# Kernel optimization log

Measured on AMD Instinct MI355X. Metric: run time of the kernel, lower is better.

Reference implementation:

```python
import jax, jax.numpy as jnp
import numpy as np

BN_EPS = 1e-5
W_SCALE = 0.05  # keep pre-softmax logits in a sane range with random weights


def setup_inputs() -> dict:
    key = jax.random.key(0)
    ks = jax.random.split(key, 8)
    b, C, H, W = 2, 512, 80, 80
    Ck, Cv, Co = 256, 256, 512
    return {
        "x": jax.random.normal(ks[0], (b, C, H, W), dtype=jnp.float32),
        "wk": jax.random.normal(ks[1], (Ck, C), dtype=jnp.float32) * W_SCALE,
        "bk": jax.random.normal(ks[2], (Ck,), dtype=jnp.float32) * W_SCALE,
        "gamma": jnp.ones((Ck,), dtype=jnp.float32),
        "beta": jnp.zeros((Ck,), dtype=jnp.float32),
        "rmean": jnp.zeros((Ck,), dtype=jnp.float32),
        "rvar": jnp.ones((Ck,), dtype=jnp.float32),
        "wv": jax.random.normal(ks[3], (Cv, C), dtype=jnp.float32) * W_SCALE,
        "bv": jax.random.normal(ks[4], (Cv,), dtype=jnp.float32) * W_SCALE,
        "wW": jax.random.normal(ks[5], (Co, Cv), dtype=jnp.float32) * W_SCALE,
        "bW": jax.random.normal(ks[6], (Co,), dtype=jnp.float32) * W_SCALE,
    }


def reference(x, wk, bk, gamma, beta, rmean, rvar, wv, bv, wW, bW):
    b, C, H, Wd = x.shape
    N = H * Wd
    Ck = wk.shape[0]
    Cv = wv.shape[0]
    # f_key == f_query (shared module): 1x1 conv + BN(inference) + ReLU
    k = jnp.einsum('bchw,oc->bohw', x, wk) + bk[:, None, None]
    scale_bn = gamma / jnp.sqrt(rvar + BN_EPS)
    k = (k - rmean[:, None, None]) * scale_bn[:, None, None] + beta[:, None, None]
    k = jax.nn.relu(k).reshape(b, Ck, N)          # [b, Ck, N]
    q = jnp.transpose(k, (0, 2, 1))               # [b, N, Ck] (query shares weights with key)
    # f_value: plain 1x1 conv
    v = (jnp.einsum('bchw,oc->bohw', x, wv) + bv[:, None, None]).reshape(b, Cv, N)
    sim = jnp.einsum('bnc,bcm->bnm', q, k) * (Ck ** -0.5)  # [b, N, N]
    sim = jax.nn.softmax(sim, axis=-1)
    ctx = jnp.einsum('bnm,bvm->bvn', sim, v).reshape(b, Cv, H, Wd)
    out = jnp.einsum('bvhw,ov->bohw', ctx, wW) + bW[:, None, None]
    return out
```

## Files before the change

kernel.cpp:

```cpp
#include <hip/hip_runtime.h>
#include <stdint.h>

typedef __attribute__((ext_vector_type(8))) short bf16x8;
typedef __attribute__((ext_vector_type(4))) float f32x4;

__device__ __forceinline__ ushort f2bf(float f) {
    union { float f; uint32_t i; } v; v.f = f;
    uint32_t r = v.i + 0x7fff + ((v.i >> 16) & 1);
    return (ushort)(r >> 16);
}
__device__ __forceinline__ uint32_t cvtpk(float lo, float hi) {
    uint32_t r;
    asm("v_cvt_pk_bf16_f32 %0, %1, %2" : "=v"(r) : "v"(lo), "v"(hi));
    return r;
}

typedef unsigned int uint_as1 __attribute__((address_space(1)));
typedef unsigned int uint_as3 __attribute__((address_space(3)));
__device__ __forceinline__ void async16(const void* g, void* l) {
    __builtin_amdgcn_global_load_lds((const uint_as1*)g, (uint_as3*)l, 16, 0, 0);
}


__global__ void cvt_f32_bf16(const float* __restrict__ in, ushort* __restrict__ out, int n) {
    int i = blockIdx.x * blockDim.x + threadIdx.x;
    if (i < n) out[i] = f2bf(in[i]);
}

__global__ void prep_bn(const float* __restrict__ bk, const float* __restrict__ gamma,
                        const float* __restrict__ beta, const float* __restrict__ rmean,
                        const float* __restrict__ rvar,
                        float* __restrict__ scaleA, float* __restrict__ shiftA) {
    int i = threadIdx.x;
    float s = gamma[i] * rsqrtf(rvar[i] + 1e-5f);
    scaleA[i] = 0.25f * s;
    shiftA[i] = 0.25f * ((bk[i] - rmean[i]) * s + beta[i]);
}

__global__ void transpose_cvt(const float* __restrict__ x, ushort* __restrict__ xt) {
    __shared__ float t[32][33];
    int b = blockIdx.z;
    int n0 = blockIdx.x * 32, c0 = blockIdx.y * 32;
    const float* xb = x + (size_t)b * 512 * 6400;
    ushort* xtb = xt + (size_t)b * 6400 * 512;
    int tx = threadIdx.x, ty = threadIdx.y;
    t[ty][tx] = xb[(size_t)(c0 + ty) * 6400 + n0 + tx];
    __syncthreads();
    xtb[(size_t)(n0 + ty) * 512 + c0 + tx] = f2bf(t[tx][ty]);
}

template <int EPI>
__global__ __launch_bounds__(256) void gemm_nt(
    const ushort* __restrict__ A, const ushort* __restrict__ B, void* __restrict__ Cout,
    int K, int lda, int ldb, int ldc,
    size_t zsa, size_t zsb, size_t zsc,
    const float* __restrict__ vec0, const float* __restrict__ vec1) {
    __shared__ __align__(16) ushort smem[6 * 4096];

    A += (size_t)blockIdx.z * zsa;
    B += (size_t)blockIdx.z * zsb;

    const int tid = threadIdx.x;
    const int lane = tid & 63, wave = tid >> 6;
    const int wm = wave & 1, wn = wave >> 1;
    const int bM = blockIdx.y * 128, bN = blockIdx.x * 128;

    const int sr = lane >> 2;
    const int sc = (lane & 3) * 8;
    const ushort* gA0 = A + (size_t)(bM + wave * 32 + sr) * lda + sc;
    const ushort* gA1 = gA0 + (size_t)16 * lda;
    const ushort* gB0 = B + (size_t)(bN + wave * 32 + sr) * ldb + sc;
    const ushort* gB1 = gB0 + (size_t)16 * ldb;
    ushort* lAw = &smem[wave * 1024];
    ushort* lBw = &smem[3 * 4096 + wave * 1024];

    const int rowA = wm * 64;
    const int rowB = wn * 64;
    const int fr = lane & 15;
    const int fk = (lane >> 4) * 8;

    f32x4 acc[4][4] = {};
    const int nT = K >> 5;

    auto stage = [&](int t, int buf) {
        const int k0 = t * 32;
        const int ob = buf * 4096;
        async16(gA0 + k0, lAw + ob);
        async16(gA1 + k0, lAw + ob + 512);
        async16(gB0 + k0, lBw + ob);
        async16(gB1 + k0, lBw + ob + 512);
    };

    stage(0, 0);
    if (nT > 1) stage(1, 1);

    for (int t = 0; t < nT; ++t) {
        if (t + 1 < nT) { asm volatile("s_waitcnt vmcnt(4)" ::: "memory"); }
        else            { asm volatile("s_waitcnt vmcnt(0)" ::: "memory"); }
        __builtin_amdgcn_sched_barrier(0);
        __builtin_amdgcn_s_barrier();
        __builtin_amdgcn_sched_barrier(0);
        if (t + 2 < nT) stage(t + 2, (t + 2) % 3);
        const int cur = t % 3;
        const ushort* lA = &smem[cur * 4096];
        const ushort* lB = &smem[3 * 4096 + cur * 4096];
        bf16x8 af[4], bff[4];
#pragma unroll
        for (int mi = 0; mi < 4; mi++)
            af[mi] = *(const bf16x8*)&lA[(rowA + mi * 16 + fr) * 32 + fk];
#pragma unroll
        for (int ni = 0; ni < 4; ni++)
            bff[ni] = *(const bf16x8*)&lB[(rowB + ni * 16 + fr) * 32 + fk];
#pragma unroll
        for (int mi = 0; mi < 4; mi++)
#pragma unroll
            for (int ni = 0; ni < 4; ni++)
                acc[mi][ni] = __builtin_amdgcn_mfma_f32_16x16x32_bf16(af[mi], bff[ni], acc[mi][ni], 0, 0, 0);
        __builtin_amdgcn_sched_barrier(0);
    }
    __builtin_amdgcn_s_barrier();
    __builtin_amdgcn_sched_barrier(0);

    float* Cf = (float*)Cout + (size_t)blockIdx.z * zsc;
    ushort* Cu = (ushort*)Cout + (size_t)blockIdx.z * zsc;
    float* lt = (float*)smem;
    const int g4 = (lane >> 4) * 4;
    const int cl = lane & 15;
    const int lr = tid >> 3;
    const int ch = tid & 7;

#pragma unroll
    for (int mi = 0; mi < 4; ++mi) {
#pragma unroll
        for (int ni = 0; ni < 4; ++ni) {
            const int lcol = wn * 64 + ni * 16 + cl;
#pragma unroll
            for (int r = 0; r < 4; ++r)
                lt[(wm * 16 + g4 + r) * 132 + lcol] = acc[mi][ni][r];
        }
        __syncthreads();
        {
            const int brow = (lr < 16) ? (mi * 16 + lr) : (64 + mi * 16 + (lr - 16));
            const int grow = bM + brow;
            const int gcol = bN + ch * 16;
            float vv[16];
#pragma unroll
            for (int i = 0; i < 16; i += 4) {
                f32x4 q = *(const f32x4*)&lt[lr * 132 + ch * 16 + i];
                vv[i] = q[0]; vv[i + 1] = q[1]; vv[i + 2] = q[2]; vv[i + 3] = q[3];
            }
            if (EPI == 1) {
#pragma unroll
                for (int i = 0; i < 16; i++)
                    vv[i] = fmaxf(vv[i] * vec0[gcol + i] + vec1[gcol + i], 0.f);
            }
            if (EPI == 2 || EPI == 3) {
                const float rb = vec0[grow];
#pragma unroll
                for (int i = 0; i < 16; i++) vv[i] += rb;
            }
            if (EPI == 3) {
#pragma unroll
                for (int i = 0; i < 16; i += 4) {
                    f32x4 q = { vv[i], vv[i + 1], vv[i + 2], vv[i + 3] };
                    *(f32x4*)&Cf[(size_t)grow * ldc + gcol + i] = q;
                }
            } else {
                uint4 q0 = { cvtpk(vv[0], vv[1]), cvtpk(vv[2], vv[3]),
                             cvtpk(vv[4], vv[5]), cvtpk(vv[6], vv[7]) };
                uint4 q1 = { cvtpk(vv[8], vv[9]), cvtpk(vv[10], vv[11]),
                             cvtpk(vv[12], vv[13]), cvtpk(vv[14], vv[15]) };
                *(uint4*)&Cu[(size_t)grow * ldc + gcol] = q0;
                *(uint4*)&Cu[(size_t)grow * ldc + gcol + 8] = q1;
            }
        }
        __syncthreads();
    }
}

template <int EPI>
__global__ __launch_bounds__(256) void gemm_wide(
    const ushort* __restrict__ A, const ushort* __restrict__ B, void* __restrict__ Cout,
    int K, int lda, int ldb, int ldc,
    size_t zsa, size_t zsb, size_t zsc,
    float* __restrict__ rsum) {
    __shared__ __align__(16) ushort smem[3 * 4096 + 3 * 8192];

    A += (size_t)blockIdx.z * zsa;
    B += (size_t)blockIdx.z * zsb;

    const int tid = threadIdx.x;
    const int lane = tid & 63, wave = tid >> 6;
    const int wm = wave & 1, wn = wave >> 1;
    const int bM = blockIdx.y * 128, bN = blockIdx.x * 256;

    const int sr = lane >> 2;
    const int scs = ((lane & 3) ^ ((lane >> 3) & 3)) * 8;
    const ushort* gA0 = A + (size_t)(bM + wave * 32 + sr) * lda + scs;
    const ushort* gA1 = gA0 + (size_t)16 * lda;
    const ushort* gB0 = B + (size_t)(bN + wave * 64 + sr) * ldb + scs;
    const ushort* gB1 = gB0 + (size_t)16 * ldb;
    const ushort* gB2 = gB0 + (size_t)32 * ldb;
    const ushort* gB3 = gB0 + (size_t)48 * ldb;
    ushort* lAw = &smem[wave * 1024];
    ushort* lBw = &smem[3 * 4096 + wave * 2048];

    const int rowA = wm * 64;
    const int rowB = wn * 128;
    const int fr = lane & 15;
    const int fq = lane >> 4;
    const int fk = (fq ^ ((fr >> 1) & 3)) * 8;

    f32x4 acc[4][8] = {};
    const int nT = K >> 5;

    auto stage = [&](int t, int buf) {
        const int k0 = t * 32;
        ushort* la = lAw + buf * 4096;
        ushort* lb = lBw + buf * 8192;
        async16(gA0 + k0, la);
        async16(gA1 + k0, la + 512);
        async16(gB0 + k0, lb);
        async16(gB1 + k0, lb + 512);
        async16(gB2 + k0, lb + 1024);
        async16(gB3 + k0, lb + 1536);
    };

    stage(0, 0);
    if (nT > 1) stage(1, 1);

    for (int t = 0; t < nT; ++t) {
        if (t + 1 < nT) { asm volatile("s_waitcnt vmcnt(6)" ::: "memory"); }
        else            { asm volatile("s_waitcnt vmcnt(0)" ::: "memory"); }
        __builtin_amdgcn_sched_barrier(0);
        __builtin_amdgcn_s_barrier();
        __builtin_amdgcn_sched_barrier(0);
        if (t + 2 < nT) stage(t + 2, (t + 2) % 3);
        const int cur = t % 3;
        const ushort* lA = &smem[cur * 4096];
        const ushort* lB = &smem[3 * 4096 + cur * 8192];
        bf16x8 af[4], bff[8];
#pragma unroll
        for (int mi = 0; mi < 4; mi++)
            af[mi] = *(const bf16x8*)&lA[(rowA + mi * 16 + fr) * 32 + fk];
#pragma unroll
        for (int ni = 0; ni < 8; ni++)
            bff[ni] = *(const bf16x8*)&lB[(rowB + ni * 16 + fr) * 32 + fk];
#pragma unroll
        for (int mi = 0; mi < 4; mi++)
#pragma unroll
            for (int ni = 0; ni < 8; ni++)
                acc[mi][ni] = __builtin_amdgcn_mfma_f32_16x16x32_bf16(af[mi], bff[ni], acc[mi][ni], 0, 0, 0);
        __builtin_amdgcn_sched_barrier(0);
    }
    __builtin_amdgcn_s_barrier();
    __builtin_amdgcn_sched_barrier(0);

    float* Cf = (float*)Cout + (size_t)blockIdx.z * zsc;
    ushort* Cu = (ushort*)Cout + (size_t)blockIdx.z * zsc;
    float* lt = (float*)smem;
    const int g4 = fq * 4;
    const int cl = fr;
    const int lr = tid >> 3;
    const int ch = tid & 7;

#pragma unroll
    for (int mi = 0; mi < 4; ++mi) {
#pragma unroll
        for (int ni = 0; ni < 8; ++ni) {
            const int lcol = wn * 128 + ni * 16 + cl;
#pragma unroll
            for (int r = 0; r < 4; ++r)
                lt[(wm * 16 + g4 + r) * 260 + lcol] = acc[mi][ni][r];
        }
        __syncthreads();
        {
            const int brow = (lr < 16) ? (mi * 16 + lr) : (64 + mi * 16 + (lr - 16));
            const int grow = bM + brow;
            float vv[32];
#pragma unroll
            for (int h = 0; h < 2; ++h)
#pragma unroll
                for (int i = 0; i < 16; i += 4) {
                    f32x4 q = *(const f32x4*)&lt[lr * 260 + h * 128 + ch * 16 + i];
                    vv[h * 16 + i] = q[0]; vv[h * 16 + i + 1] = q[1];
                    vv[h * 16 + i + 2] = q[2]; vv[h * 16 + i + 3] = q[3];
                }
            if (EPI == 5) {
                float ssum = 0.f;
#pragma unroll
                for (int i = 0; i < 32; i++) { vv[i] = __expf(vv[i]); ssum += vv[i]; }
                ssum += __shfl_down(ssum, 4, 8);
                ssum += __shfl_down(ssum, 2, 8);
                ssum += __shfl_down(ssum, 1, 8);
                if (ch == 0) rsum[(size_t)blockIdx.x * 6400 + grow] = ssum;
#pragma unroll
                for (int h = 0; h < 2; ++h) {
                    const int gcol = bN + h * 128 + ch * 16;
                    const float* p = &vv[h * 16];
                    uint4 q0 = { cvtpk(p[0], p[1]), cvtpk(p[2], p[3]),
                                 cvtpk(p[4], p[5]), cvtpk(p[6], p[7]) };
                    uint4 q1 = { cvtpk(p[8], p[9]), cvtpk(p[10], p[11]),
                                 cvtpk(p[12], p[13]), cvtpk(p[14], p[15]) };
                    *(uint4*)&Cu[(size_t)grow * ldc + gcol] = q0;
                    *(uint4*)&Cu[(size_t)grow * ldc + gcol + 8] = q1;
                }
            } else {
#pragma unroll
                for (int h = 0; h < 2; ++h) {
                    const int gcol = bN + h * 128 + ch * 16;
#pragma unroll
                    for (int i = 0; i < 16; i += 4) {
                        f32x4 q = { vv[h * 16 + i], vv[h * 16 + i + 1],
                                    vv[h * 16 + i + 2], vv[h * 16 + i + 3] };
                        *(f32x4*)&Cf[(size_t)grow * ldc + gcol + i] = q;
                    }
                }
            }
        }
        __syncthreads();
    }
}

__global__ __launch_bounds__(256) void combine_inv(const float* __restrict__ rsum,
                                                   float* __restrict__ inv) {
    int r = blockIdx.x * 256 + threadIdx.x;
    float s = 0.f;
#pragma unroll
    for (int xb = 0; xb < 25; xb++) s += rsum[(size_t)xb * 6400 + r];
    inv[r] = 1.f / s;
}

__global__ __launch_bounds__(256) void reduce_ctx(const float* __restrict__ part, ushort* __restrict__ ctx,
                                                  const float* __restrict__ inv) {
    const size_t CH = 1638400;
    size_t i = ((size_t)blockIdx.x * 256 + threadIdx.x) * 4;
    float4 a = *(const float4*)&part[i];
#pragma unroll
    for (int c = 1; c < 10; c++) {
        float4 s = *(const float4*)&part[i + (size_t)c * CH];
        a.x += s.x; a.y += s.y; a.z += s.z; a.w += s.w;
    }
    const float w = inv[i >> 8];
    uint2 o = { cvtpk(a.x * w, a.y * w), cvtpk(a.z * w, a.w * w) };
    *(uint2*)&ctx[i] = o;
}

extern "C" void kernel_launch(void* const* d_in, const int* in_sizes, int n_in,
                              void* d_out, int out_size, void* d_ws, size_t ws_size,
                              hipStream_t stream) {
    (void)in_sizes; (void)n_in; (void)out_size; (void)ws_size;
    const float* x     = (const float*)d_in[0];
    const float* wk    = (const float*)d_in[1];
    const float* bk    = (const float*)d_in[2];
    const float* gamma = (const float*)d_in[3];
    const float* beta  = (const float*)d_in[4];
    const float* rmean = (const float*)d_in[5];
    const float* rvar  = (const float*)d_in[6];
    const float* wv    = (const float*)d_in[7];
    const float* bv    = (const float*)d_in[8];
    const float* wW    = (const float*)d_in[9];
    const float* bW    = (const float*)d_in[10];
    float* out = (float*)d_out;

    ushort* Xt   = (ushort*)d_ws;
    ushort* wkb  = Xt + 6553600;
    ushort* wvb  = wkb + 131072;
    ushort* wWb  = wvb + 131072;
    ushort* Kt   = wWb + 131072;
    ushort* V    = Kt + 3276800;
    ushort* ctxT = V + 3276800;
    ushort* S    = ctxT + 3276800;
    float* scaleA = (float*)(S + 40960000);
    float* shiftA = scaleA + 256;
    float* rowsum = shiftA + 256;
    float* inv    = rowsum + 160000;
    float* part   = inv + 6400;

    cvt_f32_bf16<<<512, 256, 0, stream>>>(wk, wkb, 131072);
    cvt_f32_bf16<<<512, 256, 0, stream>>>(wv, wvb, 131072);
    cvt_f32_bf16<<<512, 256, 0, stream>>>(wW, wWb, 131072);
    prep_bn<<<1, 256, 0, stream>>>(bk, gamma, beta, rmean, rvar, scaleA, shiftA);
    transpose_cvt<<<dim3(200, 16, 2), dim3(32, 32), 0, stream>>>(x, Xt);

    gemm_nt<1><<<dim3(2, 50, 2), 256, 0, stream>>>(Xt, wkb, Kt, 512, 512, 512, 256,
                                                   3276800, 0, 1638400, scaleA, shiftA);
    gemm_nt<2><<<dim3(50, 2, 2), 256, 0, stream>>>(wvb, Xt, V, 512, 512, 512, 6400,
                                                   0, 3276800, 1638400, bv, nullptr);

    for (int b = 0; b < 2; b++) {
        ushort* Ktb  = Kt + (size_t)b * 1638400;
        ushort* Vb   = V  + (size_t)b * 1638400;
        ushort* ctxb = ctxT + (size_t)b * 1638400;
        gemm_wide<5><<<dim3(25, 50), 256, 0, stream>>>(Ktb, Ktb, S, 256, 256, 256, 6400,
                                                       0, 0, 0, rowsum);
        combine_inv<<<25, 256, 0, stream>>>(rowsum, inv);
        gemm_wide<4><<<dim3(1, 50, 10), 256, 0, stream>>>(S, Vb, part, 640, 6400, 6400, 256,
                                                          640, 640, 1638400, nullptr);
        reduce_ctx<<<1600, 256, 0, stream>>>(part, ctxb, inv);
    }

    gemm_nt<3><<<dim3(50, 4, 2), 256, 0, stream>>>(wWb, ctxT, out, 256, 256, 256, 6400,
                                                   0, 1638400, 3276800, bW, nullptr);
}
```

Measured before the change: 338.1 us.

## Fuse QK^T, exp and PV into one flash-style kernel, drop S buffer

New measurement: 312.5 us. 7.6% less time.

```diff
diff --git a/kernel.cpp b/kernel.cpp
--- a/kernel.cpp
+++ b/kernel.cpp
@@ -66,10 +66,10 @@
     const int bM = blockIdx.y * 128, bN = blockIdx.x * 128;
 
     const int sr = lane >> 2;
-    const int sc = (lane & 3) * 8;
-    const ushort* gA0 = A + (size_t)(bM + wave * 32 + sr) * lda + sc;
+    const int scs = ((lane & 3) ^ ((lane >> 3) & 3)) * 8;
+    const ushort* gA0 = A + (size_t)(bM + wave * 32 + sr) * lda + scs;
     const ushort* gA1 = gA0 + (size_t)16 * lda;
-    const ushort* gB0 = B + (size_t)(bN + wave * 32 + sr) * ldb + sc;
+    const ushort* gB0 = B + (size_t)(bN + wave * 32 + sr) * ldb + scs;
     const ushort* gB1 = gB0 + (size_t)16 * ldb;
     ushort* lAw = &smem[wave * 1024];
     ushort* lBw = &smem[3 * 4096 + wave * 1024];
@@ -77,7 +77,7 @@
     const int rowA = wm * 64;
     const int rowB = wn * 64;
     const int fr = lane & 15;
-    const int fk = (lane >> 4) * 8;
+    const int fk = ((lane >> 4) ^ ((fr >> 1) & 3)) * 8;
 
     f32x4 acc[4][4] = {};
     const int nT = K >> 5;
@@ -178,147 +178,208 @@
     }
 }
 
-template <int EPI>
-__global__ __launch_bounds__(256) void gemm_wide(
-    const ushort* __restrict__ A, const ushort* __restrict__ B, void* __restrict__ Cout,
-    int K, int lda, int ldb, int ldc,
-    size_t zsa, size_t zsb, size_t zsc,
+__global__ __launch_bounds__(256, 2) void fused_spv(
+    const ushort* __restrict__ Kt,
+    const ushort* __restrict__ V,
+    float* __restrict__ part,
     float* __restrict__ rsum) {
-    __shared__ __align__(16) ushort smem[3 * 4096 + 3 * 8192];
-
-    A += (size_t)blockIdx.z * zsa;
-    B += (size_t)blockIdx.z * zsb;
+    __shared__ __align__(16) ushort smem[40960];
+
+    const ushort* Ktb = Kt + (size_t)blockIdx.z * 1638400;
+    const ushort* Vb  = V  + (size_t)blockIdx.z * 1638400;
+    float* partb = part + (size_t)blockIdx.z * 8192000;
+    float* rsumb = rsum + (size_t)blockIdx.z * 32000;
 
     const int tid = threadIdx.x;
     const int lane = tid & 63, wave = tid >> 6;
     const int wm = wave & 1, wn = wave >> 1;
-    const int bM = blockIdx.y * 128, bN = blockIdx.x * 256;
+    const int mc = blockIdx.x;
+    const int bM = blockIdx.y * 128;
 
     const int sr = lane >> 2;
     const int scs = ((lane & 3) ^ ((lane >> 3) & 3)) * 8;
-    const ushort* gA0 = A + (size_t)(bM + wave * 32 + sr) * lda + scs;
-    const ushort* gA1 = gA0 + (size_t)16 * lda;
-    const ushort* gB0 = B + (size_t)(bN + wave * 64 + sr) * ldb + scs;
-    const ushort* gB1 = gB0 + (size_t)16 * ldb;
-    const ushort* gB2 = gB0 + (size_t)32 * ldb;
-    const ushort* gB3 = gB0 + (size_t)48 * ldb;
+    const ushort* gA0 = Ktb + (size_t)(bM + wave * 32 + sr) * 256 + scs;
+    const ushort* gA1 = gA0 + (size_t)16 * 256;
+    const ushort* gV  = Vb + (size_t)(wave * 64 + sr) * 6400 + scs;
+
     ushort* lAw = &smem[wave * 1024];
-    ushort* lBw = &smem[3 * 4096 + wave * 2048];
-
-    const int rowA = wm * 64;
-    const int rowB = wn * 128;
+    ushort* lBw = &smem[3 * 4096 + wave * 1024];
+    ushort* Pb  = &smem[24576];
+
     const int fr = lane & 15;
     const int fq = lane >> 4;
     const int fk = (fq ^ ((fr >> 1) & 3)) * 8;
-
-    f32x4 acc[4][8] = {};
-    const int nT = K >> 5;
-
-    auto stage = [&](int t, int buf) {
-        const int k0 = t * 32;
-        ushort* la = lAw + buf * 4096;
-        ushort* lb = lBw + buf * 8192;
-        async16(gA0 + k0, la);
-        async16(gA1 + k0, la + 512);
-        async16(gB0 + k0, lb);
-        async16(gB1 + k0, lb + 512);
-        async16(gB2 + k0, lb + 1024);
-        async16(gB3 + k0, lb + 1536);
-    };
-
-    stage(0, 0);
-    if (nT > 1) stage(1, 1);
-
-    for (int t = 0; t < nT; ++t) {
-        if (t + 1 < nT) { asm volatile("s_waitcnt vmcnt(6)" ::: "memory"); }
-        else            { asm volatile("s_waitcnt vmcnt(0)" ::: "memory"); }
-        __builtin_amdgcn_sched_barrier(0);
-        __builtin_amdgcn_s_barrier();
-        __builtin_amdgcn_sched_barrier(0);
-        if (t + 2 < nT) stage(t + 2, (t + 2) % 3);
-        const int cur = t % 3;
-        const ushort* lA = &smem[cur * 4096];
-        const ushort* lB = &smem[3 * 4096 + cur * 8192];
-        bf16x8 af[4], bff[8];
-#pragma unroll
-        for (int mi = 0; mi < 4; mi++)
-            af[mi] = *(const bf16x8*)&lA[(rowA + mi * 16 + fr) * 32 + fk];
-#pragma unroll
-        for (int ni = 0; ni < 8; ni++)
-            bff[ni] = *(const bf16x8*)&lB[(rowB + ni * 16 + fr) * 32 + fk];
-#pragma unroll
-        for (int mi = 0; mi < 4; mi++)
-#pragma unroll
-            for (int ni = 0; ni < 8; ni++)
-                acc[mi][ni] = __builtin_amdgcn_mfma_f32_16x16x32_bf16(af[mi], bff[ni], acc[mi][ni], 0, 0, 0);
-        __builtin_amdgcn_sched_barrier(0);
-    }
-    __builtin_amdgcn_s_barrier();
-    __builtin_amdgcn_sched_barrier(0);
-
-    float* Cf = (float*)Cout + (size_t)blockIdx.z * zsc;
-    ushort* Cu = (ushort*)Cout + (size_t)blockIdx.z * zsc;
-    float* lt = (float*)smem;
+    const int rowA = wm * 64, rowB = wn * 64;
+
     const int g4 = fq * 4;
     const int cl = fr;
     const int lr = tid >> 3;
     const int ch = tid & 7;
-
+    const int brow_r = (lr < 16) ? lr : (64 + lr - 16);
+
+    f32x4 ctx[4][8] = {};
+    float rs0 = 0.f, rs1 = 0.f, rs2 = 0.f, rs3 = 0.f;
+
+#pragma unroll 1
+    for (int s = 0; s < 10; ++s) {
+        const int m0 = mc * 1280 + s * 128;
+        const ushort* gB0 = Ktb + (size_t)(m0 + wave * 32 + sr) * 256 + scs;
+        const ushort* gB1 = gB0 + (size_t)16 * 256;
+
+        f32x4 sac[4][4] = {};
+        auto stage = [&](int t, int buf) {
+            const int k0 = t * 32;
+            const int ob = buf * 4096;
+            async16(gA0 + k0, lAw + ob);
+            async16(gA1 + k0, lAw + ob + 512);
+            async16(gB0 + k0, lBw + ob);
+            async16(gB1 + k0, lBw + ob + 512);
+        };
+        stage(0, 0);
+        stage(1, 1);
+        for (int t = 0; t < 8; ++t) {
+            if (t < 7) { asm volatile("s_waitcnt vmcnt(4)" ::: "memory"); }
+            else       { asm volatile("s_waitcnt vmcnt(0)" ::: "memory"); }
+            __builtin_amdgcn_sched_barrier(0);
+            __builtin_amdgcn_s_barrier();
+            __builtin_amdgcn_sched_barrier(0);
+            if (t + 2 < 8) stage(t + 2, (t + 2) % 3);
+            const int cur = t % 3;
+            const ushort* lA = &smem[cur * 4096];
+            const ushort* lB = &smem[3 * 4096 + cur * 4096];
+            bf16x8 af[4], bff[4];
+#pragma unroll
+            for (int mi = 0; mi < 4; mi++)
+                af[mi] = *(const bf16x8*)&lA[(rowA + mi * 16 + fr) * 32 + fk];
+#pragma unroll
+            for (int ni = 0; ni < 4; ni++)
+                bff[ni] = *(const bf16x8*)&lB[(rowB + ni * 16 + fr) * 32 + fk];
+#pragma unroll
+            for (int mi = 0; mi < 4; mi++)
+#pragma unroll
+                for (int ni = 0; ni < 4; ni++)
+                    sac[mi][ni] = __builtin_amdgcn_mfma_f32_16x16x32_bf16(af[mi], bff[ni], sac[mi][ni], 0, 0, 0);
+            __builtin_amdgcn_sched_barrier(0);
+        }
+        __builtin_amdgcn_s_barrier();
+        __builtin_amdgcn_sched_barrier(0);
+
+        {
+            float* lt = (float*)smem;
+#pragma unroll
+            for (int mi = 0; mi < 4; ++mi) {
+#pragma unroll
+                for (int ni = 0; ni < 4; ++ni) {
+                    const int lcol = wn * 64 + ni * 16 + cl;
+#pragma unroll
+                    for (int r = 0; r < 4; ++r)
+                        lt[(wm * 16 + g4 + r) * 132 + lcol] = sac[mi][ni][r];
+                }
+                __syncthreads();
+                {
+                    const int brow = mi * 16 + brow_r;
+                    float vv[16];
+                    float ss = 0.f;
+#pragma unroll
+                    for (int i = 0; i < 16; i += 4) {
+                        f32x4 q = *(const f32x4*)&lt[lr * 132 + ch * 16 + i];
+                        vv[i] = __expf(q[0]); vv[i + 1] = __expf(q[1]);
+                        vv[i + 2] = __expf(q[2]); vv[i + 3] = __expf(q[3]);
+                        ss += vv[i] + vv[i + 1] + vv[i + 2] + vv[i + 3];
+                    }
+                    if (mi == 0) rs0 += ss; else if (mi == 1) rs1 += ss;
+                    else if (mi == 2) rs2 += ss; else rs3 += ss;
+                    const int kt = ch >> 1;
+                    const int sw = (brow >> 1) & 3;
+                    const int q0 = ((ch & 1) * 2) ^ sw;
+                    const int q1 = ((ch & 1) * 2 + 1) ^ sw;
+                    uint4 pk0 = { cvtpk(vv[0], vv[1]), cvtpk(vv[2], vv[3]),
+                                  cvtpk(vv[4], vv[5]), cvtpk(vv[6], vv[7]) };
+                    uint4 pk1 = { cvtpk(vv[8], vv[9]), cvtpk(vv[10], vv[11]),
+                                  cvtpk(vv[12], vv[13]), cvtpk(vv[14], vv[15]) };
+                    *(uint4*)&Pb[kt * 4096 + brow * 32 + q0 * 8] = pk0;
+                    *(uint4*)&Pb[kt * 4096 + brow * 32 + q1 * 8] = pk1;
+                }
+                __syncthreads();
+            }
+        }
+
+        auto stageV = [&](int t, int p) {
+            const ushort* g = gV + (size_t)(m0 + t * 32);
+            ushort* l = &smem[p * 8192 + wave * 2048];
+            async16(g, l);
+            async16(g + (size_t)16 * 6400, l + 512);
+            async16(g + (size_t)32 * 6400, l + 1024);
+            async16(g + (size_t)48 * 6400, l + 1536);
+        };
+        stageV(0, 0);
+        stageV(1, 1);
+        for (int t = 0; t < 4; ++t) {
+            if (t < 3) { asm volatile("s_waitcnt vmcnt(4)" ::: "memory"); }
+            else       { asm volatile("s_waitcnt vmcnt(0)" ::: "memory"); }
+            __builtin_amdgcn_sched_barrier(0);
+            __builtin_amdgcn_s_barrier();
+            __builtin_amdgcn_sched_barrier(0);
+            if (t + 2 < 4) stageV(t + 2, (t + 2) % 3);
+            const ushort* lV = &smem[(t % 3) * 8192];
+            bf16x8 pa[4], vf[8];
+#pragma unroll
+            for (int mi = 0; mi < 4; mi++)
+                pa[mi] = *(const bf16x8*)&Pb[t * 4096 + (rowA + mi * 16 + fr) * 32 + fk];
+#pragma unroll
+            for (int ni = 0; ni < 8; ni++)
+                vf[ni] = *(const bf16x8*)&lV[(wn * 128 + ni * 16 + fr) * 32 + fk];
+#pragma unroll
+            for (int mi = 0; mi < 4; mi++)
+#pragma unroll
+                for (int ni = 0; ni < 8; ni++)
+                    ctx[mi][ni] = __builtin_amdgcn_mfma_f32_16x16x32_bf16(pa[mi], vf[ni], ctx[mi][ni], 0, 0, 0);
+            __builtin_amdgcn_sched_barrier(0);
+        }
+        __builtin_amdgcn_s_barrier();
+        __builtin_amdgcn_sched_barrier(0);
+    }
+
+    {
+        float rsv0 = rs0, rsv1 = rs1, rsv2 = rs2, rsv3 = rs3;
+#pragma unroll
+        for (int o = 4; o > 0; o >>= 1) {
+            rsv0 += __shfl_down(rsv0, o, 8);
+            rsv1 += __shfl_down(rsv1, o, 8);
+            rsv2 += __shfl_down(rsv2, o, 8);
+            rsv3 += __shfl_down(rsv3, o, 8);
+        }
+        if (ch == 0) {
+            rsumb[(size_t)mc * 6400 + bM + 0 * 16 + brow_r] = rsv0;
+            rsumb[(size_t)mc * 6400 + bM + 1 * 16 + brow_r] = rsv1;
+            rsumb[(size_t)mc * 6400 + bM + 2 * 16 + brow_r] = rsv2;
+            rsumb[(size_t)mc * 6400 + bM + 3 * 16 + brow_r] = rsv3;
+        }
+    }
+
+    float* lt = (float*)smem;
+    float* Cf = partb + (size_t)mc * 1638400;
 #pragma unroll
     for (int mi = 0; mi < 4; ++mi) {
+        __syncthreads();
 #pragma unroll
         for (int ni = 0; ni < 8; ++ni) {
             const int lcol = wn * 128 + ni * 16 + cl;
 #pragma unroll
             for (int r = 0; r < 4; ++r)
-                lt[(wm * 16 + g4 + r) * 260 + lcol] = acc[mi][ni][r];
+                lt[(wm * 16 + g4 + r) * 260 + lcol] = ctx[mi][ni][r];
         }
         __syncthreads();
-        {
-            const int brow = (lr < 16) ? (mi * 16 + lr) : (64 + mi * 16 + (lr - 16));
-            const int grow = bM + brow;
-            float vv[32];
-#pragma unroll
-            for (int h = 0; h < 2; ++h)
-#pragma unroll
-                for (int i = 0; i < 16; i += 4) {
-                    f32x4 q = *(const f32x4*)&lt[lr * 260 + h * 128 + ch * 16 + i];
-                    vv[h * 16 + i] = q[0]; vv[h * 16 + i + 1] = q[1];
-                    vv[h * 16 + i + 2] = q[2]; vv[h * 16 + i + 3] = q[3];
-                }
-            if (EPI == 5) {
-                float ssum = 0.f;
-#pragma unroll
-                for (int i = 0; i < 32; i++) { vv[i] = __expf(vv[i]); ssum += vv[i]; }
-                ssum += __shfl_down(ssum, 4, 8);
-                ssum += __shfl_down(ssum, 2, 8);
-                ssum += __shfl_down(ssum, 1, 8);
-                if (ch == 0) rsum[(size_t)blockIdx.x * 6400 + grow] = ssum;
-#pragma unroll
-                for (int h = 0; h < 2; ++h) {
-                    const int gcol = bN + h * 128 + ch * 16;
-                    const float* p = &vv[h * 16];
-                    uint4 q0 = { cvtpk(p[0], p[1]), cvtpk(p[2], p[3]),
-                                 cvtpk(p[4], p[5]), cvtpk(p[6], p[7]) };
-                    uint4 q1 = { cvtpk(p[8], p[9]), cvtpk(p[10], p[11]),
-                                 cvtpk(p[12], p[13]), cvtpk(p[14], p[15]) };
-                    *(uint4*)&Cu[(size_t)grow * ldc + gcol] = q0;
-                    *(uint4*)&Cu[(size_t)grow * ldc + gcol + 8] = q1;
-                }
-            } else {
-#pragma unroll
-                for (int h = 0; h < 2; ++h) {
-                    const int gcol = bN + h * 128 + ch * 16;
-#pragma unroll
-                    for (int i = 0; i < 16; i += 4) {
-                        f32x4 q = { vv[h * 16 + i], vv[h * 16 + i + 1],
-                                    vv[h * 16 + i + 2], vv[h * 16 + i + 3] };
-                        *(f32x4*)&Cf[(size_t)grow * ldc + gcol + i] = q;
-                    }
-                }
-            }
-        }
-        __syncthreads();
+        const int grow = bM + mi * 16 + brow_r;
+#pragma unroll
+        for (int h = 0; h < 2; ++h) {
+            const int gcol = h * 128 + ch * 16;
+#pragma unroll
+            for (int i = 0; i < 16; i += 4) {
+                f32x4 q = *(const f32x4*)&lt[lr * 260 + gcol + i];
+                *(f32x4*)&Cf[(size_t)grow * 256 + gcol + i] = q;
+            }
+        }
     }
 }
 
@@ -327,7 +388,7 @@
     int r = blockIdx.x * 256 + threadIdx.x;
     float s = 0.f;
 #pragma unroll
-    for (int xb = 0; xb < 25; xb++) s += rsum[(size_t)xb * 6400 + r];
+    for (int xb = 0; xb < 5; xb++) s += rsum[(size_t)xb * 6400 + r];
     inv[r] = 1.f / s;
 }
 
@@ -337,7 +398,7 @@
     size_t i = ((size_t)blockIdx.x * 256 + threadIdx.x) * 4;
     float4 a = *(const float4*)&part[i];
 #pragma unroll
-    for (int c = 1; c < 10; c++) {
+    for (int c = 1; c < 5; c++) {
         float4 s = *(const float4*)&part[i + (size_t)c * CH];
         a.x += s.x; a.y += s.y; a.z += s.z; a.w += s.w;
     }
@@ -370,11 +431,10 @@
     ushort* Kt   = wWb + 131072;
     ushort* V    = Kt + 3276800;
     ushort* ctxT = V + 3276800;
-    ushort* S    = ctxT + 3276800;
-    float* scaleA = (float*)(S + 40960000);
+    float* scaleA = (float*)(ctxT + 3276800);
     float* shiftA = scaleA + 256;
     float* rowsum = shiftA + 256;
-    float* inv    = rowsum + 160000;
+    float* inv    = rowsum + 64000;
     float* part   = inv + 6400;
 
     cvt_f32_bf16<<<512, 256, 0, stream>>>(wk, wkb, 131072);
@@ -388,16 +448,12 @@
     gemm_nt<2><<<dim3(50, 2, 2), 256, 0, stream>>>(wvb, Xt, V, 512, 512, 512, 6400,
                                                    0, 3276800, 1638400, bv, nullptr);
 
+    fused_spv<<<dim3(5, 50, 2), 256, 0, stream>>>(Kt, V, part, rowsum);
+
     for (int b = 0; b < 2; b++) {
-        ushort* Ktb  = Kt + (size_t)b * 1638400;
-        ushort* Vb   = V  + (size_t)b * 1638400;
-        ushort* ctxb = ctxT + (size_t)b * 1638400;
-        gemm_wide<5><<<dim3(25, 50), 256, 0, stream>>>(Ktb, Ktb, S, 256, 256, 256, 6400,
-                                                       0, 0, 0, rowsum);
-        combine_inv<<<25, 256, 0, stream>>>(rowsum, inv);
-        gemm_wide<4><<<dim3(1, 50, 10), 256, 0, stream>>>(S, Vb, part, 640, 6400, 6400, 256,
-                                                          640, 640, 1638400, nullptr);
-        reduce_ctx<<<1600, 256, 0, stream>>>(part, ctxb, inv);
+        combine_inv<<<25, 256, 0, stream>>>(rowsum + (size_t)b * 32000, inv);
+        reduce_ctx<<<1600, 256, 0, stream>>>(part + (size_t)b * 8192000,
+                                             ctxT + (size_t)b * 1638400, inv);
     }
 
     gemm_nt<3><<<dim3(50, 4, 2), 256, 0, stream>>>(wWb, ctxT, out, 256, 256, 256, 6400,
```
